# Performance work log

Measured on AMD Instinct MI355X. Metric: run time of the kernel, lower is better.

The kernel has to match this reference:

```python
import jax, jax.numpy as jnp
import numpy as np

B, S, D, H = 8, 1024, 1024, 16
HD = D // H
EPS = 1e-5

def layernorm(x, g, b):
    mu = jnp.mean(x, axis=-1, keepdims=True)
    var = jnp.mean(jnp.square(x - mu), axis=-1, keepdims=True)
    return (x - mu) * jax.lax.rsqrt(var + EPS) * g + b

def setup_inputs() -> dict:
    key = jax.random.key(0)
    ks = jax.random.split(key, 8)
    s = 0.02
    return {
        "x": jax.random.normal(ks[0], (B, S, D), jnp.float32),
        "mask": jnp.tril(jnp.ones((S, S), jnp.int32)),  # causal mask
        "ln1_g": jnp.ones((D,), jnp.float32),
        "ln1_b": jnp.zeros((D,), jnp.float32),
        "wqkv": jax.random.normal(ks[1], (D, 3 * D), jnp.float32) * s,
        "bqkv": jnp.zeros((3 * D,), jnp.float32),
        "wo": jax.random.normal(ks[2], (D, D), jnp.float32) * s,
        "bo": jnp.zeros((D,), jnp.float32),
        "ln2_g": jnp.ones((D,), jnp.float32),
        "ln2_b": jnp.zeros((D,), jnp.float32),
        "w1": jax.random.normal(ks[3], (D, 4 * D), jnp.float32) * s,
        "b1": jnp.zeros((4 * D,), jnp.float32),
        "w2": jax.random.normal(ks[4], (4 * D, D), jnp.float32) * s,
        "b2": jnp.zeros((D,), jnp.float32),
    }

def reference(x, mask, ln1_g, ln1_b, wqkv, bqkv, wo, bo, ln2_g, ln2_b, w1, b1, w2, b2):
    # --- pre-LN attention ---
    h = layernorm(x, ln1_g, ln1_b)
    qkv = h @ wqkv + bqkv                                  # [B,S,3D]
    qkv = qkv.reshape(B, S, 3, H, HD).transpose(2, 0, 3, 1, 4)
    q, k, v = qkv[0], qkv[1], qkv[2]                       # [B,H,S,HD]
    scores = jnp.einsum('bhqd,bhkd->bhqk', q, k) / jnp.sqrt(jnp.float32(HD))
    scores = jnp.where(mask == 0, -jnp.inf, scores)
    attn = jax.nn.softmax(scores, axis=-1)
    out = jnp.einsum('bhqk,bhkd->bhqd', attn, v)           # [B,H,S,HD]
    out = out.transpose(0, 2, 1, 3).reshape(B, S, D)
    x = x + (out @ wo + bo)
    # --- pre-LN MLP ---
    h = layernorm(x, ln2_g, ln2_b)
    h = jax.nn.gelu(h @ w1 + b1, approximate=False)
    x = x + (h @ w2 + b2)
    return x
```

## Files before the change

kernel.cpp:

```cpp
#include <hip/hip_runtime.h>


#define DEV static __device__ __forceinline__

typedef __attribute__((ext_vector_type(8))) __bf16 bf16x8;
typedef __attribute__((ext_vector_type(4))) float f32x4;

DEV ushort f2bf(float f) {
  union { float f; unsigned u; } c; c.f = f;
  unsigned r = (c.u + 0x7FFFu + ((c.u >> 16) & 1u)) >> 16;
  return (ushort)r;
}

DEV float geluf(float v) {
  return 0.5f * v * (1.0f + erff(v * 0.70710678118654752f));
}

DEV void gload16(const ushort* g, ushort* l) {
  __builtin_amdgcn_global_load_lds(
      (const __attribute__((address_space(1))) void*)g,
      (__attribute__((address_space(3))) void*)l, 16, 0, 0);
}

__global__ __launch_bounds__(256)
void ln_bf16_kernel(const float* __restrict__ x, const float* __restrict__ g,
                    const float* __restrict__ bb, ushort* __restrict__ out)
{
  const int row = blockIdx.x, tid = threadIdx.x;
  const float4 v = ((const float4*)x)[row * 256 + tid];
  float s = v.x + v.y + v.z + v.w;
  float sq = v.x * v.x + v.y * v.y + v.z * v.z + v.w * v.w;
#pragma unroll
  for (int off = 32; off >= 1; off >>= 1) {
    s += __shfl_xor(s, off, 64);
    sq += __shfl_xor(sq, off, 64);
  }
  __shared__ float ps[4], pq[4];
  if ((tid & 63) == 0) { ps[tid >> 6] = s; pq[tid >> 6] = sq; }
  __syncthreads();
  s = ps[0] + ps[1] + ps[2] + ps[3];
  sq = pq[0] + pq[1] + pq[2] + pq[3];
  const float mu = s * (1.0f / 1024.0f);
  const float rstd = rsqrtf(sq * (1.0f / 1024.0f) - mu * mu + 1e-5f);
  const float4 gv = ((const float4*)g)[tid];
  const float4 bv = ((const float4*)bb)[tid];
  ushort4 o;
  o.x = f2bf((v.x - mu) * rstd * gv.x + bv.x);
  o.y = f2bf((v.y - mu) * rstd * gv.y + bv.y);
  o.z = f2bf((v.z - mu) * rstd * gv.z + bv.z);
  o.w = f2bf((v.w - mu) * rstd * gv.w + bv.w);
  ((ushort4*)out)[row * 256 + tid] = o;
}

__global__ __launch_bounds__(256)
void tcvt_kernel(const float* __restrict__ in, ushort* __restrict__ out, int K, int N)
{
  __shared__ float tile[32][33];
  const int tx = threadIdx.x & 31, ty = threadIdx.x >> 5;
  const int n0 = blockIdx.x * 32, k0 = blockIdx.y * 32;
#pragma unroll
  for (int j = 0; j < 4; ++j)
    tile[ty + j * 8][tx] = in[(size_t)(k0 + ty + j * 8) * N + n0 + tx];
  __syncthreads();
#pragma unroll
  for (int j = 0; j < 4; ++j)
    out[(size_t)(n0 + ty + j * 8) * K + k0 + tx] = f2bf(tile[tx][ty + j * 8]);
}

__global__ __launch_bounds__(256)
void vtr_kernel(const ushort* __restrict__ qkv, ushort* __restrict__ VT)
{
  __shared__ ushort tile[64][72];
  const int tid = threadIdx.x;
  const int bh = blockIdx.x, sb = blockIdx.y;
  const int b = bh >> 4, h = bh & 15;
  const int s0 = sb * 64;
#pragma unroll
  for (int it = 0; it < 2; ++it) {
    const int idx = it * 256 + tid;
    const int r = idx >> 3, hc = (idx & 7) * 8;
    *(int4*)&tile[r][hc] =
        *(const int4*)(qkv + ((size_t)b * 1024 + s0 + r) * 3072 + 2048 + h * 64 + hc);
  }
  __syncthreads();
#pragma unroll
  for (int it = 0; it < 2; ++it) {
    const int idx = it * 256 + tid;
    const int hd = idx >> 3, sc = (idx & 7) * 8;
    union { int4 v; ushort u[8]; } o;
#pragma unroll
    for (int j = 0; j < 8; ++j) o.u[j] = tile[sc + j][hd];
    *(int4*)(VT + ((size_t)bh * 64 + hd) * 1024 + s0 + sc) = o.v;
  }
}

template<int EPI>
__global__ __launch_bounds__(256)
void gemm_bf16(const ushort* __restrict__ A, const ushort* __restrict__ Bt,
               const float* __restrict__ bias, const float* __restrict__ resid,
               void* __restrict__ outp, int M, int N, int K)
{
  __shared__ ushort Asl[128 * 64];
  __shared__ ushort Bsl[128 * 64];
  const int tid = threadIdx.x;
  const int lane = tid & 63, w = tid >> 6;
  const int wm = w >> 1, wn = w & 1;
  const int grp = lane >> 4, r16 = lane & 15;
  const int bm = blockIdx.y * 128, bn = blockIdx.x * 128;

  const int lrow = lane >> 3;
  const int uswz = ((lane & 7) ^ lrow) * 8;
  const ushort* pa = A  + (size_t)(bm + w * 32 + lrow) * K + uswz;
  const ushort* pb = Bt + (size_t)(bn + w * 32 + lrow) * K + uswz;

  f32x4 acc[4][4] = {};

  for (int k0 = 0; k0 < K; k0 += 64) {
    __syncthreads();
#pragma unroll
    for (int i = 0; i < 4; ++i) {
      gload16(pa + (size_t)(i * 8) * K + k0, &Asl[(w * 32 + i * 8) * 64]);
      gload16(pb + (size_t)(i * 8) * K + k0, &Bsl[(w * 32 + i * 8) * 64]);
    }
    __syncthreads();
#pragma unroll
    for (int ks = 0; ks < 2; ++ks) {
      bf16x8 af[4], bfr[4];
#pragma unroll
      for (int m = 0; m < 4; ++m) {
        const int r = wm * 64 + m * 16 + r16;
        af[m] = *(const bf16x8*)&Asl[r * 64 + ((ks * 4 + grp) ^ (r16 & 7)) * 8];
      }
#pragma unroll
      for (int n = 0; n < 4; ++n) {
        const int r = wn * 64 + n * 16 + r16;
        bfr[n] = *(const bf16x8*)&Bsl[r * 64 + ((ks * 4 + grp) ^ (r16 & 7)) * 8];
      }
#pragma unroll
      for (int m = 0; m < 4; ++m)
#pragma unroll
        for (int n = 0; n < 4; ++n)
          acc[m][n] = __builtin_amdgcn_mfma_f32_16x16x32_bf16(af[m], bfr[n], acc[m][n], 0, 0, 0);
    }
  }

#pragma unroll
  for (int n = 0; n < 4; ++n) {
    const int col = bn + wn * 64 + n * 16 + r16;
    const float bval = bias[col];
#pragma unroll
    for (int m = 0; m < 4; ++m) {
      const int row0 = bm + wm * 64 + m * 16 + grp * 4;
#pragma unroll
      for (int r = 0; r < 4; ++r) {
        const size_t idx = (size_t)(row0 + r) * N + col;
        float v = acc[m][n][r] + bval;
        if (EPI == 1) v = geluf(v);
        if (EPI == 2) ((float*)outp)[idx] = v + resid[idx];
        else          ((ushort*)outp)[idx] = f2bf(v);
      }
    }
  }
}

__global__ __launch_bounds__(256)
void attn_kernel(const ushort* __restrict__ qkv, const ushort* __restrict__ VT,
                 ushort* __restrict__ out)
{
  __shared__ ushort Ks[64 * 64];
  __shared__ ushort Vs[64 * 64];
  __shared__ ushort Ps[4][16][72];
  const int tid = threadIdx.x, lane = tid & 63, w = tid >> 6;
  const int grp = lane >> 4, r16 = lane & 15;
  const int qb = 15 - blockIdx.x;
  const int bh = blockIdx.y;
  const int b = bh >> 4, h = bh & 15;
  const size_t rowbase = (size_t)b * 1024;
  const int q0 = qb * 64 + w * 16;

  bf16x8 qf[2];
  {
    const ushort* qp = qkv + (rowbase + q0 + r16) * 3072 + h * 64;
    qf[0] = *(const bf16x8*)(qp + grp * 8);
    qf[1] = *(const bf16x8*)(qp + 32 + grp * 8);
  }

  const int lrow = lane >> 3;
  const int uswz = ((lane & 7) ^ lrow) * 8;
  const ushort* kstg = qkv + (rowbase + w * 16 + lrow) * 3072 + 1024 + h * 64 + uswz;
  const ushort* vstg = VT + ((size_t)bh * 64 + w * 16 + lrow) * 1024 + uswz;

  f32x4 o[4] = {};
  float mrow[4] = {-1e30f, -1e30f, -1e30f, -1e30f};
  float lsum[4] = {0.f, 0.f, 0.f, 0.f};

  for (int kb = 0; kb <= qb; ++kb) {
    __syncthreads();
#pragma unroll
    for (int i = 0; i < 2; ++i) {
      gload16(kstg + (size_t)(kb * 64 + i * 8) * 3072, &Ks[(w * 16 + i * 8) * 64]);
      gload16(vstg + (size_t)(i * 8) * 1024 + kb * 64, &Vs[(w * 16 + i * 8) * 64]);
    }
    __syncthreads();

    f32x4 s[4] = {};
#pragma unroll
    for (int t = 0; t < 4; ++t) {
      const int r = t * 16 + r16;
#pragma unroll
      for (int f = 0; f < 2; ++f) {
        const bf16x8 kf = *(const bf16x8*)&Ks[r * 64 + ((f * 4 + grp) ^ (r16 & 7)) * 8];
        s[t] = __builtin_amdgcn_mfma_f32_16x16x32_bf16(qf[f], kf, s[t], 0, 0, 0);
      }
    }
#pragma unroll
    for (int t = 0; t < 4; ++t)
#pragma unroll
      for (int r = 0; r < 4; ++r) {
        float v = s[t][r] * 0.125f;
        if (kb == qb && (t * 16 + r16) > (w * 16 + grp * 4 + r)) v = -1e30f;
        s[t][r] = v;
      }
    float fac[4];
#pragma unroll
    for (int r = 0; r < 4; ++r) {
      float mx = fmaxf(fmaxf(s[0][r], s[1][r]), fmaxf(s[2][r], s[3][r]));
#pragma unroll
      for (int msk = 1; msk < 16; msk <<= 1) mx = fmaxf(mx, __shfl_xor(mx, msk, 16));
      const float mn = fmaxf(mrow[r], mx);
      fac[r] = __expf(mrow[r] - mn);
      mrow[r] = mn;
      lsum[r] *= fac[r];
    }
#pragma unroll
    for (int t = 0; t < 4; ++t)
#pragma unroll
      for (int r = 0; r < 4; ++r) o[t][r] *= fac[r];
    float rsum[4] = {0.f, 0.f, 0.f, 0.f};
#pragma unroll
    for (int t = 0; t < 4; ++t)
#pragma unroll
      for (int r = 0; r < 4; ++r) {
        const float p = __expf(s[t][r] - mrow[r]);
        s[t][r] = p;
        rsum[r] += p;
      }
#pragma unroll
    for (int r = 0; r < 4; ++r) {
#pragma unroll
      for (int msk = 1; msk < 16; msk <<= 1) rsum[r] += __shfl_xor(rsum[r], msk, 16);
      lsum[r] += rsum[r];
    }
#pragma unroll
    for (int t = 0; t < 4; ++t)
#pragma unroll
      for (int r = 0; r < 4; ++r)
        Ps[w][grp * 4 + r][t * 16 + r16] = f2bf(s[t][r]);
    bf16x8 pf[2];
    pf[0] = *(const bf16x8*)&Ps[w][r16][grp * 8];
    pf[1] = *(const bf16x8*)&Ps[w][r16][32 + grp * 8];
#pragma unroll
    for (int t = 0; t < 4; ++t) {
      const int r = t * 16 + r16;
#pragma unroll
      for (int f = 0; f < 2; ++f) {
        const bf16x8 vf = *(const bf16x8*)&Vs[r * 64 + ((f * 4 + grp) ^ (r16 & 7)) * 8];
        o[t] = __builtin_amdgcn_mfma_f32_16x16x32_bf16(pf[f], vf, o[t], 0, 0, 0);
      }
    }
  }

  float inv[4];
#pragma unroll
  for (int r = 0; r < 4; ++r) inv[r] = 1.0f / lsum[r];
#pragma unroll
  for (int t = 0; t < 4; ++t)
#pragma unroll
    for (int r = 0; r < 4; ++r) {
      const int qrow = qb * 64 + w * 16 + grp * 4 + r;
      out[(rowbase + qrow) * 1024 + h * 64 + t * 16 + r16] = f2bf(o[t][r] * inv[r]);
    }
}

extern "C" void kernel_launch(void* const* d_in, const int* in_sizes, int n_in,
                              void* d_out, int out_size, void* d_ws, size_t ws_size,
                              hipStream_t stream) {
  (void)in_sizes; (void)n_in; (void)out_size; (void)ws_size;
  const float* x     = (const float*)d_in[0];
  const float* ln1_g = (const float*)d_in[2];
  const float* ln1_b = (const float*)d_in[3];
  const float* wqkv  = (const float*)d_in[4];
  const float* bqkv  = (const float*)d_in[5];
  const float* wo    = (const float*)d_in[6];
  const float* bo    = (const float*)d_in[7];
  const float* ln2_g = (const float*)d_in[8];
  const float* ln2_b = (const float*)d_in[9];
  const float* w1    = (const float*)d_in[10];
  const float* b1    = (const float*)d_in[11];
  const float* w2    = (const float*)d_in[12];
  const float* b2    = (const float*)d_in[13];
  float* out = (float*)d_out;
  char* ws = (char*)d_ws;

  ushort* wqkvT = (ushort*)(ws + 0);
  ushort* woT   = (ushort*)(ws + 6291456);
  ushort* w1T   = (ushort*)(ws + 8388608);
  ushort* w2T   = (ushort*)(ws + 16777216);
  ushort* R1    = (ushort*)(ws + 25165824);
  ushort* R2    = (ushort*)(ws + 41943040);
  ushort* VT    = (ushort*)(ws + 41943040 + 50331648);

  const dim3 blk(256);
  tcvt_kernel<<<dim3(3072 / 32, 1024 / 32), blk, 0, stream>>>(wqkv, wqkvT, 1024, 3072);
  tcvt_kernel<<<dim3(1024 / 32, 1024 / 32), blk, 0, stream>>>(wo, woT, 1024, 1024);
  tcvt_kernel<<<dim3(4096 / 32, 1024 / 32), blk, 0, stream>>>(w1, w1T, 1024, 4096);
  tcvt_kernel<<<dim3(1024 / 32, 4096 / 32), blk, 0, stream>>>(w2, w2T, 4096, 1024);

  ln_bf16_kernel<<<8192, blk, 0, stream>>>(x, ln1_g, ln1_b, R1);
  gemm_bf16<0><<<dim3(3072 / 128, 8192 / 128), blk, 0, stream>>>(R1, wqkvT, bqkv, nullptr, R2, 8192, 3072, 1024);
  vtr_kernel<<<dim3(128, 16), blk, 0, stream>>>(R2, VT);
  attn_kernel<<<dim3(16, 128), blk, 0, stream>>>(R2, VT, R1);
  gemm_bf16<2><<<dim3(1024 / 128, 8192 / 128), blk, 0, stream>>>(R1, woT, bo, x, out, 8192, 1024, 1024);
  ln_bf16_kernel<<<8192, blk, 0, stream>>>(out, ln2_g, ln2_b, R1);
  gemm_bf16<1><<<dim3(4096 / 128, 8192 / 128), blk, 0, stream>>>(R1, w1T, b1, nullptr, R2, 8192, 4096, 1024);
  gemm_bf16<2><<<dim3(1024 / 128, 8192 / 128), blk, 0, stream>>>(R2, w2T, b2, out, out, 8192, 1024, 4096);
}
```

Baseline: 551.1 us.

## Add 256x256-tile double-buffered GEMM for QKV and MLP-up projections

Adds a new bf16 GEMM kernel with 256x256 output tiles, 512 threads and 128KB of dynamic LDS. It double-buffers K-tiles with direct global-to-LDS loads, swizzles LDS addresses to avoid bank conflicts and raises wave priority around the MFMA blocks. It is used for the QKV and first MLP GEMMs, to raise arithmetic intensity and overlap loads with compute. The trade-off is larger per-block resources, fewer blocks per grid (384 and 512), and a possible tail effect on 256 CUs.

```diff
diff --git a/kernel.cpp b/kernel.cpp
--- a/kernel.cpp
+++ b/kernel.cpp
@@ -158,6 +158,100 @@
         if (EPI == 1) v = geluf(v);
         if (EPI == 2) ((float*)outp)[idx] = v + resid[idx];
         else          ((ushort*)outp)[idx] = f2bf(v);
+      }
+    }
+  }
+}
+
+template<int EPI>
+__global__ __launch_bounds__(512, 2)
+void gemm256(const ushort* __restrict__ A, const ushort* __restrict__ Bt,
+             const float* __restrict__ bias, void* __restrict__ outp,
+             int M, int N, int K)
+{
+  extern __shared__ ushort sm[];
+  const int tid = threadIdx.x;
+  const int lane = tid & 63, w = tid >> 6;
+  const int wm = w >> 2, wn = w & 3;
+  const int grp = lane >> 4, r16 = lane & 15;
+  const int bm = blockIdx.y * 256, bn = blockIdx.x * 256;
+
+  const int lrow = lane >> 3;
+  const int uswz = ((lane & 7) ^ lrow) * 8;
+  const ushort* pa = A  + (size_t)(bm + w * 32 + lrow) * K + uswz;
+  const ushort* pb = Bt + (size_t)(bn + w * 32 + lrow) * K + uswz;
+
+  const int nt = K >> 6;
+  f32x4 acc[8][4] = {};
+
+#pragma unroll
+  for (int i = 0; i < 4; ++i) {
+    gload16(pa + (size_t)(i * 8) * K, &sm[(w * 32 + i * 8) * 64]);
+    gload16(pb + (size_t)(i * 8) * K, &sm[16384 + (w * 32 + i * 8) * 64]);
+  }
+#pragma unroll
+  for (int i = 0; i < 4; ++i) {
+    gload16(pa + (size_t)(i * 8) * K + 64, &sm[32768 + (w * 32 + i * 8) * 64]);
+    gload16(pb + (size_t)(i * 8) * K + 64, &sm[32768 + 16384 + (w * 32 + i * 8) * 64]);
+  }
+
+  for (int t = 0; t < nt; ++t) {
+    if (t + 1 < nt) { asm volatile("s_waitcnt vmcnt(8)" ::: "memory"); }
+    else            { asm volatile("s_waitcnt vmcnt(0)" ::: "memory"); }
+    __builtin_amdgcn_s_barrier();
+    __builtin_amdgcn_sched_barrier(0);
+    const ushort* as = sm + (t & 1) * 32768;
+    const ushort* bs = as + 16384;
+#pragma unroll
+    for (int ks = 0; ks < 2; ++ks) {
+      bf16x8 af[8], bfr[4];
+#pragma unroll
+      for (int mf = 0; mf < 8; ++mf) {
+        const int r = wm * 128 + mf * 16 + r16;
+        af[mf] = *(const bf16x8*)&as[r * 64 + ((ks * 4 + grp) ^ (r16 & 7)) * 8];
+      }
+#pragma unroll
+      for (int nf = 0; nf < 4; ++nf) {
+        const int r = wn * 64 + nf * 16 + r16;
+        bfr[nf] = *(const bf16x8*)&bs[r * 64 + ((ks * 4 + grp) ^ (r16 & 7)) * 8];
+      }
+      __builtin_amdgcn_s_setprio(1);
+#pragma unroll
+      for (int mf = 0; mf < 8; ++mf)
+#pragma unroll
+        for (int nf = 0; nf < 4; ++nf)
+          acc[mf][nf] = __builtin_amdgcn_mfma_f32_16x16x32_bf16(af[mf], bfr[nf], acc[mf][nf], 0, 0, 0);
+      __builtin_amdgcn_s_setprio(0);
+    }
+    asm volatile("s_waitcnt lgkmcnt(0)" ::: "memory");
+    __builtin_amdgcn_sched_barrier(0);
+    __builtin_amdgcn_s_barrier();
+    __builtin_amdgcn_sched_barrier(0);
+    if (t + 2 < nt) {
+      const int k0 = (t + 2) * 64;
+      ushort* za = sm + (t & 1) * 32768;
+      ushort* zb = za + 16384;
+#pragma unroll
+      for (int i = 0; i < 4; ++i) {
+        gload16(pa + (size_t)(i * 8) * K + k0, &za[(w * 32 + i * 8) * 64]);
+        gload16(pb + (size_t)(i * 8) * K + k0, &zb[(w * 32 + i * 8) * 64]);
+      }
+    }
+  }
+
+#pragma unroll
+  for (int nf = 0; nf < 4; ++nf) {
+    const int col = bn + wn * 64 + nf * 16 + r16;
+    const float bval = bias[col];
+#pragma unroll
+    for (int mf = 0; mf < 8; ++mf) {
+      const int row0 = bm + wm * 128 + mf * 16 + grp * 4;
+#pragma unroll
+      for (int r = 0; r < 4; ++r) {
+        const size_t idx = (size_t)(row0 + r) * N + col;
+        float v = acc[mf][nf][r] + bval;
+        if (EPI == 1) v = geluf(v);
+        ((ushort*)outp)[idx] = f2bf(v);
       }
     }
   }
@@ -310,6 +404,11 @@
   ushort* R2    = (ushort*)(ws + 41943040);
   ushort* VT    = (ushort*)(ws + 41943040 + 50331648);
 
+  hipFuncSetAttribute(reinterpret_cast<const void*>(gemm256<0>),
+                      hipFuncAttributeMaxDynamicSharedMemorySize, 131072);
+  hipFuncSetAttribute(reinterpret_cast<const void*>(gemm256<1>),
+                      hipFuncAttributeMaxDynamicSharedMemorySize, 131072);
+
   const dim3 blk(256);
   tcvt_kernel<<<dim3(3072 / 32, 1024 / 32), blk, 0, stream>>>(wqkv, wqkvT, 1024, 3072);
   tcvt_kernel<<<dim3(1024 / 32, 1024 / 32), blk, 0, stream>>>(wo, woT, 1024, 1024);
@@ -317,11 +416,11 @@
   tcvt_kernel<<<dim3(1024 / 32, 4096 / 32), blk, 0, stream>>>(w2, w2T, 4096, 1024);
 
   ln_bf16_kernel<<<8192, blk, 0, stream>>>(x, ln1_g, ln1_b, R1);
-  gemm_bf16<0><<<dim3(3072 / 128, 8192 / 128), blk, 0, stream>>>(R1, wqkvT, bqkv, nullptr, R2, 8192, 3072, 1024);
+  gemm256<0><<<dim3(3072 / 256, 8192 / 256), 512, 131072, stream>>>(R1, wqkvT, bqkv, R2, 8192, 3072, 1024);
   vtr_kernel<<<dim3(128, 16), blk, 0, stream>>>(R2, VT);
   attn_kernel<<<dim3(16, 128), blk, 0, stream>>>(R2, VT, R1);
   gemm_bf16<2><<<dim3(1024 / 128, 8192 / 128), blk, 0, stream>>>(R1, woT, bo, x, out, 8192, 1024, 1024);
   ln_bf16_kernel<<<8192, blk, 0, stream>>>(out, ln2_g, ln2_b, R1);
-  gemm_bf16<1><<<dim3(4096 / 128, 8192 / 128), blk, 0, stream>>>(R1, w1T, b1, nullptr, R2, 8192, 4096, 1024);
+  gemm256<1><<<dim3(4096 / 256, 8192 / 256), 512, 131072, stream>>>(R1, w1T, b1, R2, 8192, 4096, 1024);
   gemm_bf16<2><<<dim3(1024 / 128, 8192 / 128), blk, 0, stream>>>(R2, w2T, b2, out, out, 8192, 1024, 4096);
 }
```

Result: slower. 578.3 us (+4.9%).
